# Kernel optimization log

Measured on AMD Instinct MI355X. Metric: run time of the kernel, lower is better.

Reference implementation:

```python
import jax, jax.numpy as jnp
import numpy as np

N_SRC = 50000
N_DST = 50000
E = 800000
D = 128
K = 8  # args.k: number of randomly sampled neighbors


def setup_inputs() -> dict:
    key = jax.random.key(0)
    k1, k2, k3, k4, k5, k6 = jax.random.split(key, 6)
    h_src = jax.random.normal(k1, (N_SRC, D), dtype=jnp.float32)
    h_dst = jax.random.normal(k2, (N_DST, D), dtype=jnp.float32)
    unif = jax.random.uniform(k3, (N_DST, K), dtype=jnp.float32)
    src_idx = jax.random.randint(k4, (E,), 0, N_SRC, dtype=jnp.int32)
    dst_idx = jnp.sort(jax.random.randint(k5, (E,), 0, N_DST, dtype=jnp.int32))
    category = jax.random.randint(k6, (N_SRC,), 0, 50, dtype=jnp.int32)
    return {"h_src": h_src, "h_dst": h_dst, "unif": unif,
            "src_idx": src_idx, "dst_idx": dst_idx, "category": category}


def _forward(h_src, h_dst, unif, src_idx, dst_idx, category):
    n_src = h_src.shape[0]
    n_dst = h_dst.shape[0]
    e = src_idx.shape[0]
    ones = jnp.ones((e,), dtype=h_src.dtype)

    # src-side symmetric norm: feat_src * out_deg^-0.5
    out_deg = jax.ops.segment_sum(ones, src_idx, num_segments=n_src)
    out_norm = jnp.clip(out_deg, 1.0, None) ** -0.5
    feat_src = h_src * out_norm[:, None]

    # mailbox gather: message per edge m_e = feat_src[src_e]  -> [E, D]
    msg = feat_src[src_idx]

    # in-degrees and full segment-sum reduction
    in_deg = jax.ops.segment_sum(ones, dst_idx, num_segments=n_dst)
    full_sum = jax.ops.segment_sum(msg, dst_idx, num_segments=n_dst)  # [N_dst, D]

    # random neighbor subsampling with replacement (dst_idx is sorted):
    # node n owns edges [ptr[n], ptr[n]+deg[n]); pick K offsets via floor(u*deg)
    deg_i = in_deg.astype(jnp.int32)
    ptr = jnp.searchsorted(dst_idx, jnp.arange(n_dst, dtype=jnp.int32), side="left").astype(jnp.int32)
    off = jnp.floor(unif * in_deg[:, None]).astype(jnp.int32)
    off = jnp.minimum(off, jnp.maximum(deg_i[:, None] - 1, 0))  # guard u==1 / deg==0
    eid = jnp.clip(ptr[:, None] + off, 0, e - 1)                # [N_dst, K]
    samp_sum = msg[eid].sum(axis=1)                              # [N_dst, D]

    # bucket escape hatch: any incoming category == -1 -> sum everything
    neg_in = jax.ops.segment_sum((category[src_idx] == -1).astype(jnp.int32),
                                 dst_idx, num_segments=n_dst)
    use_full = (deg_i <= K) | (neg_in > 0)
    rst = jnp.where(use_full[:, None], full_sum, samp_sum)

    # dst-side norm: rst * in_deg^-0.5
    in_norm = jnp.clip(in_deg, 1.0, None) ** -0.5
    return rst * in_norm[:, None]


def reference(h_src, h_dst, unif, src_idx, dst_idx, category):
    return _forward(h_src, h_dst, unif, src_idx, dst_idx, category)
```

## Files before the change

### kernel.cpp

```cpp
#include <hip/hip_runtime.h>

#define N_SRC 50000
#define N_DST 50000
#define E_CNT 800000
#define D 128
#define K 8

#define EDGE_BLOCKS ((E_CNT + 255) / 256)
#define PTR_BLOCKS  ((N_DST + 1 + 255) / 256)


__global__ void count_ptr_kernel(const int* __restrict__ src_idx,
                                 const int* __restrict__ dst_idx,
                                 const int* __restrict__ category,
                                 int* __restrict__ out_deg,
                                 int* __restrict__ neg_in,
                                 int* __restrict__ ptr) {
    if (blockIdx.x < EDGE_BLOCKS) {
        int e = blockIdx.x * 256 + threadIdx.x;
        if (e >= E_CNT) return;
        int s = src_idx[e];
        atomicAdd(&out_deg[s], 1);
        if (category[s] == -1) {
            atomicAdd(&neg_in[dst_idx[e]], 1);
        }
    } else {
        int n = (blockIdx.x - EDGE_BLOCKS) * 256 + threadIdx.x;
        if (n > N_DST) return;
        int lo = 0, hi = E_CNT;
        while (lo < hi) {
            int mid = (lo + hi) >> 1;
            if (dst_idx[mid] < n) lo = mid + 1; else hi = mid;
        }
        ptr[n] = lo;
    }
}

__global__ void gather_kernel(const float* __restrict__ h_src,
                              const float* __restrict__ unif,
                              const int* __restrict__ src_idx,
                              const int* __restrict__ out_deg,
                              const int* __restrict__ neg_in,
                              const int* __restrict__ ptr,
                              float* __restrict__ out) {
    int gid = blockIdx.x * blockDim.x + threadIdx.x;
    int n = gid >> 6;
    int lane = threadIdx.x & 63;
    if (n >= N_DST) return;

    int p = ptr[n];
    int deg = ptr[n + 1] - p;
    bool use_full = (deg <= K) || (neg_in[n] > 0);

    const float2* h2 = (const float2*)h_src;
    float2 acc = make_float2(0.f, 0.f);

    if (use_full) {
        for (int i = 0; i < deg; ++i) {
            int s = src_idx[p + i];
            float norm = rsqrtf((float)max(out_deg[s], 1));
            float2 v = h2[(size_t)s * 64 + lane];
            acc.x += v.x * norm;
            acc.y += v.y * norm;
        }
    } else {
        int s_k = 0;
        if (lane < K) {
            float u = unif[n * K + lane];
            int off = (int)floorf(u * (float)deg);
            if (off > deg - 1) off = deg - 1;
            if (off < 0) off = 0;
            int eid = p + off;
            if (eid < 0) eid = 0;
            if (eid > E_CNT - 1) eid = E_CNT - 1;
            s_k = src_idx[eid];
        }
        #pragma unroll
        for (int k = 0; k < K; ++k) {
            int s = __shfl(s_k, k, 64);
            float norm = rsqrtf((float)max(out_deg[s], 1));
            float2 v = h2[(size_t)s * 64 + lane];
            acc.x += v.x * norm;
            acc.y += v.y * norm;
        }
    }

    float in_norm = rsqrtf((float)max(deg, 1));
    float2 r;
    r.x = acc.x * in_norm;
    r.y = acc.y * in_norm;
    ((float2*)out)[(size_t)n * 64 + lane] = r;
}

extern "C" void kernel_launch(void* const* d_in, const int* in_sizes, int n_in,
                              void* d_out, int out_size, void* d_ws, size_t ws_size,
                              hipStream_t stream) {
    const float* h_src   = (const float*)d_in[0];
    const float* unif    = (const float*)d_in[2];
    const int* src_idx   = (const int*)d_in[3];
    const int* dst_idx   = (const int*)d_in[4];
    const int* category  = (const int*)d_in[5];
    float* out = (float*)d_out;

    int* out_deg = (int*)d_ws;
    int* neg_in  = out_deg + N_SRC;
    int* ptr     = neg_in + N_DST;

    hipMemsetAsync(out_deg, 0, (size_t)(N_SRC + N_DST) * sizeof(int), stream);

    count_ptr_kernel<<<EDGE_BLOCKS + PTR_BLOCKS, 256, 0, stream>>>(
        src_idx, dst_idx, category, out_deg, neg_in, ptr);

    {
        int threads = 256;
        long long total = (long long)N_DST * 64;
        int blocks = (int)((total + threads - 1) / threads);
        gather_kernel<<<blocks, threads, 0, stream>>>(h_src, unif, src_idx,
                                                      out_deg, neg_in,
                                                      ptr, out);
    }
}
```

Before: 163.2 us.

## Privatize out-degree atomics per XCD and precompute source norms

Result: no change. 162.5 us (-0.4%).

```diff
diff --git a/kernel.cpp b/kernel.cpp
--- a/kernel.cpp
+++ b/kernel.cpp
@@ -5,27 +5,44 @@
 #define E_CNT 800000
 #define D 128
 #define K 8
+#define NSHADOW 8
 
-#define EDGE_BLOCKS ((E_CNT + 255) / 256)
-#define PTR_BLOCKS  ((N_DST + 1 + 255) / 256)
+#define CNT_THREADS (E_CNT / 4)
+#define CNT_BLOCKS ((CNT_THREADS + 255) / 256)
+#define PTR_BLOCKS ((N_DST + 1 + 255) / 256)
 
+
+__device__ __forceinline__ int xcc_id() {
+    int x;
+    asm("s_getreg_b32 %0, hwreg(HW_REG_XCC_ID)" : "=s"(x));
+    return x & (NSHADOW - 1);
+}
+
+__device__ __forceinline__ void atomic_add_xcd(int* p, int v) {
+    asm volatile("global_atomic_add %0, %1, off" :: "v"(p), "v"(v) : "memory");
+}
 
 __global__ void count_ptr_kernel(const int* __restrict__ src_idx,
                                  const int* __restrict__ dst_idx,
                                  const int* __restrict__ category,
-                                 int* __restrict__ out_deg,
+                                 int* __restrict__ shadow,
                                  int* __restrict__ neg_in,
                                  int* __restrict__ ptr) {
-    if (blockIdx.x < EDGE_BLOCKS) {
-        int e = blockIdx.x * 256 + threadIdx.x;
-        if (e >= E_CNT) return;
-        int s = src_idx[e];
-        atomicAdd(&out_deg[s], 1);
-        if (category[s] == -1) {
-            atomicAdd(&neg_in[dst_idx[e]], 1);
-        }
+    if (blockIdx.x < CNT_BLOCKS) {
+        int t = blockIdx.x * 256 + threadIdx.x;
+        if (t >= CNT_THREADS) return;
+        int* sh = shadow + (size_t)xcc_id() * N_SRC;
+        int4 s = ((const int4*)src_idx)[t];
+        atomic_add_xcd(&sh[s.x], 1);
+        atomic_add_xcd(&sh[s.y], 1);
+        atomic_add_xcd(&sh[s.z], 1);
+        atomic_add_xcd(&sh[s.w], 1);
+        if (category[s.x] == -1) atomicAdd(&neg_in[dst_idx[4 * t + 0]], 1);
+        if (category[s.y] == -1) atomicAdd(&neg_in[dst_idx[4 * t + 1]], 1);
+        if (category[s.z] == -1) atomicAdd(&neg_in[dst_idx[4 * t + 2]], 1);
+        if (category[s.w] == -1) atomicAdd(&neg_in[dst_idx[4 * t + 3]], 1);
     } else {
-        int n = (blockIdx.x - EDGE_BLOCKS) * 256 + threadIdx.x;
+        int n = (blockIdx.x - CNT_BLOCKS) * 256 + threadIdx.x;
         if (n > N_DST) return;
         int lo = 0, hi = E_CNT;
         while (lo < hi) {
@@ -36,10 +53,20 @@
     }
 }
 
+__global__ void reduce_norm_kernel(const int* __restrict__ shadow,
+                                   float* __restrict__ out_norm) {
+    int n = blockIdx.x * blockDim.x + threadIdx.x;
+    if (n >= N_SRC) return;
+    int d = 0;
+    #pragma unroll
+    for (int x = 0; x < NSHADOW; ++x) d += shadow[(size_t)x * N_SRC + n];
+    out_norm[n] = rsqrtf((float)max(d, 1));
+}
+
 __global__ void gather_kernel(const float* __restrict__ h_src,
                               const float* __restrict__ unif,
                               const int* __restrict__ src_idx,
-                              const int* __restrict__ out_deg,
+                              const float* __restrict__ out_norm,
                               const int* __restrict__ neg_in,
                               const int* __restrict__ ptr,
                               float* __restrict__ out) {
@@ -58,7 +85,7 @@
     if (use_full) {
         for (int i = 0; i < deg; ++i) {
             int s = src_idx[p + i];
-            float norm = rsqrtf((float)max(out_deg[s], 1));
+            float norm = out_norm[s];
             float2 v = h2[(size_t)s * 64 + lane];
             acc.x += v.x * norm;
             acc.y += v.y * norm;
@@ -78,7 +105,7 @@
         #pragma unroll
         for (int k = 0; k < K; ++k) {
             int s = __shfl(s_k, k, 64);
-            float norm = rsqrtf((float)max(out_deg[s], 1));
+            float norm = out_norm[s];
             float2 v = h2[(size_t)s * 64 + lane];
             acc.x += v.x * norm;
             acc.y += v.y * norm;
@@ -102,21 +129,24 @@
     const int* category  = (const int*)d_in[5];
     float* out = (float*)d_out;
 
-    int* out_deg = (int*)d_ws;
-    int* neg_in  = out_deg + N_SRC;
-    int* ptr     = neg_in + N_DST;
+    int* shadow    = (int*)d_ws;
+    int* neg_in    = shadow + (size_t)NSHADOW * N_SRC;
+    int* ptr       = neg_in + N_DST;
+    float* out_norm = (float*)(ptr + N_DST + 1);
 
-    hipMemsetAsync(out_deg, 0, (size_t)(N_SRC + N_DST) * sizeof(int), stream);
+    hipMemsetAsync(shadow, 0, ((size_t)NSHADOW * N_SRC + N_DST) * sizeof(int), stream);
 
-    count_ptr_kernel<<<EDGE_BLOCKS + PTR_BLOCKS, 256, 0, stream>>>(
-        src_idx, dst_idx, category, out_deg, neg_in, ptr);
+    count_ptr_kernel<<<CNT_BLOCKS + PTR_BLOCKS, 256, 0, stream>>>(
+        src_idx, dst_idx, category, shadow, neg_in, ptr);
+
+    reduce_norm_kernel<<<(N_SRC + 255) / 256, 256, 0, stream>>>(shadow, out_norm);
 
     {
         int threads = 256;
         long long total = (long long)N_DST * 64;
         int blocks = (int)((total + threads - 1) / threads);
         gather_kernel<<<blocks, threads, 0, stream>>>(h_src, unif, src_idx,
-                                                      out_deg, neg_in,
+                                                      out_norm, neg_in,
                                                       ptr, out);
     }
 }
```
